# Kernel tuning notes

Measured on AMD Instinct MI355X. Metric: run time of the kernel, lower is better.

Reference implementation:

```python
import jax, jax.numpy as jnp
import numpy as np
import math

B, S, D, H = 4, 2048, 1024, 16
HD = D // H  # head_size = 64


def setup_inputs() -> dict:
    key = jax.random.key(0)
    ks = jax.random.split(key, 12)
    s = 1.0 / math.sqrt(D)
    inp = {
        "query_in": jax.random.normal(ks[0], (B, S, D), jnp.float32),
        "key_in": jax.random.normal(ks[1], (B, S, D), jnp.float32),
        "values_in": jax.random.normal(ks[2], (B, S, D), jnp.float32),
        # causal mask, broadcast over batch and heads
        "mask": jnp.tril(jnp.ones((S, S), jnp.int32))[None, None],
        "Wq": jax.random.normal(ks[3], (D, D), jnp.float32) * s,
        "bq": jnp.zeros((D,), jnp.float32),
        "Wk": jax.random.normal(ks[4], (D, D), jnp.float32) * s,
        "bk": jnp.zeros((D,), jnp.float32),
        "Wv": jax.random.normal(ks[5], (D, D), jnp.float32) * s,
        "bv": jnp.zeros((D,), jnp.float32),
        "Wo": jax.random.normal(ks[6], (D, D), jnp.float32) * s,
        "bo": jnp.zeros((D,), jnp.float32),
    }
    return inp


def _heads(x):
    # [B,S,D] -> [B,H,S,HD]
    return x.reshape(B, S, H, HD).transpose(0, 2, 1, 3)


def reference(query_in, key_in, values_in, mask, Wq, bq, Wk, bk, Wv, bv, Wo, bo):
    q = _heads(query_in @ Wq.T + bq)
    k = _heads(key_in @ Wk.T + bk)
    v = _heads(values_in @ Wv.T + bv)
    # scaled dot-product scores [B,H,Sq,Sk]
    att = jnp.einsum("bhqd,bhkd->bhqk", q, k) / math.sqrt(HD)
    att = jnp.where(mask == 0, jnp.float32(-1e9), att)
    # NOTE: original module applies dropout (identity at eval / p=0) directly
    # to scores with NO softmax -- faithfully reproduced here.
    out = jnp.einsum("bhqk,bhkd->bhqd", att, v)
    out = out.transpose(0, 2, 1, 3).reshape(B, S, D)
    return out @ Wo.T + bo
```

## Files before the change

### kernel.cpp

```cpp
#include <hip/hip_runtime.h>
#include <stdint.h>

typedef unsigned short ushort_t;
typedef __bf16 bf16x8 __attribute__((ext_vector_type(8)));
typedef float f32x4 __attribute__((ext_vector_type(4)));
typedef ushort_t us4 __attribute__((ext_vector_type(4)));

#define MFMA16(a, b, c) __builtin_amdgcn_mfma_f32_16x16x32_bf16((a), (b), (c), 0, 0, 0)

constexpr int Bn = 4, Sn = 2048, Dn = 1024, Hn = 16, HDn = 64;
constexpr float SCALE = 0.125f;
constexpr float NEG = -1e9f;

__device__ __forceinline__ float bf2f(ushort_t u) {
  unsigned x = ((unsigned)u) << 16;
  return __builtin_bit_cast(float, x);
}
__device__ __forceinline__ ushort_t f2bf(float f) {
  unsigned x = __builtin_bit_cast(unsigned, f);
  x = x + 0x7FFFu + ((x >> 16) & 1u);
  return (ushort_t)(x >> 16);
}
__device__ __forceinline__ uint4 ld8_f32_bf16(const float* __restrict__ p) {
  float4 a = *(const float4*)p;
  float4 b = *(const float4*)(p + 4);
  union { ushort_t u[8]; uint4 v; } r;
  r.u[0] = f2bf(a.x); r.u[1] = f2bf(a.y); r.u[2] = f2bf(a.z); r.u[3] = f2bf(a.w);
  r.u[4] = f2bf(b.x); r.u[5] = f2bf(b.y); r.u[6] = f2bf(b.z); r.u[7] = f2bf(b.w);
  return r.v;
}
__device__ __forceinline__ void gl2lds16(const void* g, void* l) {
  __builtin_amdgcn_global_load_lds(
      (__attribute__((address_space(1))) void*)g,
      (__attribute__((address_space(3))) void*)l, 16, 0, 0);
}

__global__ __launch_bounds__(256)
void cvt_all(const float* __restrict__ xq, const float* __restrict__ xk,
             const float* __restrict__ xv, const float* __restrict__ wq,
             const float* __restrict__ wk, const float* __restrict__ wv,
             const float* __restrict__ wo, ushort_t* __restrict__ Xd,
             ushort_t* __restrict__ Wd) {
  const int bid = blockIdx.x;
  if (bid < 12288) {
    const int which = bid >> 12;
    const float* s = which == 0 ? xq : which == 1 ? xk : xv;
    size_t i = ((size_t)(bid & 4095) * 256 + threadIdx.x) * 8;
    *(uint4*)(Xd + (size_t)which * 8388608 + i) = ld8_f32_bf16(s + i);
  } else {
    const int wb = bid - 12288, which = wb >> 9;
    const float* s = which == 0 ? wq : which == 1 ? wk : which == 2 ? wv : wo;
    size_t i = ((size_t)(wb & 511) * 256 + threadIdx.x) * 8;
    *(uint4*)(Wd + (size_t)which * 1048576 + i) = ld8_f32_bf16(s + i);
  }
}

__global__ __launch_bounds__(256, 4)
void gemm_qkv(const ushort_t* __restrict__ Xb, const ushort_t* __restrict__ Wb,
              const float* __restrict__ bq, const float* __restrict__ bk,
              const float* __restrict__ bv, ushort_t* __restrict__ Qd,
              ushort_t* __restrict__ Ktd, ushort_t* __restrict__ Vtd) {
  constexpr int K = 1024;
  __shared__ __align__(16) ushort_t As[128 * 64];
  __shared__ __align__(16) ushort_t Bs[128 * 64];

  const int z = blockIdx.z;
  const ushort_t* A  = Xb + (size_t)z * 8388608;
  const ushort_t* Wt = Wb + (size_t)z * 1048576;
  const float* bias = z == 0 ? bq : z == 1 ? bk : bv;
  ushort_t* Cp = z == 0 ? Qd : z == 1 ? Ktd : Vtd;

  const int tid = threadIdx.x;
  const int lane = tid & 63, w = tid >> 6;
  const int quad = lane >> 4, l16 = lane & 15;
  const int wm = w >> 1, wn = w & 1;
  const int row0 = blockIdx.x * 128;
  const int col0 = blockIdx.y * 128;

  const int sr = lane >> 3;
  const int sg = ((lane & 7) ^ (sr & 7)) * 8;
  const ushort_t* Ab = A  + (size_t)(row0 + w * 32 + sr) * K + sg;
  const ushort_t* Bb = Wt + (size_t)(col0 + w * 32 + sr) * K + sg;

  f32x4 acc[4][4] = {};

  for (int k0 = 0; k0 < K; k0 += 64) {
    __syncthreads();
#pragma unroll
    for (int i = 0; i < 4; ++i) {
      gl2lds16(Ab + (size_t)(i * 8) * K + k0, &As[(w * 32 + i * 8) * 64]);
      gl2lds16(Bb + (size_t)(i * 8) * K + k0, &Bs[(w * 32 + i * 8) * 64]);
    }
    __syncthreads();
#pragma unroll
    for (int ks = 0; ks < 2; ++ks) {
      const int kg = ((ks * 4 + quad) ^ (l16 & 7)) * 8;
      bf16x8 af[4], bfr[4];
#pragma unroll
      for (int mt = 0; mt < 4; ++mt)
        af[mt] = *(const bf16x8*)(&As[(wm * 64 + mt * 16 + l16) * 64 + kg]);
#pragma unroll
      for (int nt = 0; nt < 4; ++nt)
        bfr[nt] = *(const bf16x8*)(&Bs[(wn * 64 + nt * 16 + l16) * 64 + kg]);
#pragma unroll
      for (int mt = 0; mt < 4; ++mt)
#pragma unroll
        for (int nt = 0; nt < 4; ++nt)
          acc[mt][nt] = MFMA16(af[mt], bfr[nt], acc[mt][nt]);
    }
  }

#pragma unroll
  for (int mt = 0; mt < 4; ++mt) {
#pragma unroll
    for (int nt = 0; nt < 4; ++nt) {
      const int col = col0 + wn * 64 + nt * 16 + l16;
      const float bv4 = bias[col];
      const int rowb = row0 + wm * 64 + mt * 16 + quad * 4;
      if (z != 0) {
        const int b = rowb >> 11, s = rowb & (Sn - 1);
        const int h = col >> 6, hd = col & 63;
        us4 pk;
#pragma unroll
        for (int r = 0; r < 4; ++r) pk[r] = f2bf(acc[mt][nt][r] + bv4);
        *(us4*)(Cp + ((size_t)((b * Hn + h) * HDn + hd)) * Sn + s) = pk;
      } else {
#pragma unroll
        for (int r = 0; r < 4; ++r) {
          const int row = rowb + r;
          const int b = row >> 11, s = row & (Sn - 1);
          const int h = col >> 6, hd = col & 63;
          Cp[(((size_t)(b * Hn + h) * Sn + s) << 6) + hd] = f2bf(acc[mt][nt][r] + bv4);
        }
      }
    }
  }
}

__global__ __launch_bounds__(256, 4)
void gemm_out(const ushort_t* __restrict__ A, const ushort_t* __restrict__ Wt,
              const float* __restrict__ bias, float* __restrict__ Cp) {
  constexpr int K = 1024;
  __shared__ __align__(16) ushort_t As[128 * 64];
  __shared__ __align__(16) ushort_t Bs[128 * 64];

  const int tid = threadIdx.x;
  const int lane = tid & 63, w = tid >> 6;
  const int quad = lane >> 4, l16 = lane & 15;
  const int wm = w >> 1, wn = w & 1;
  const int row0 = blockIdx.x * 128;
  const int col0 = blockIdx.y * 128;

  const int sr = lane >> 3;
  const int sg = ((lane & 7) ^ (sr & 7)) * 8;
  const ushort_t* Ab = A  + (size_t)(row0 + w * 32 + sr) * K + sg;
  const ushort_t* Bb = Wt + (size_t)(col0 + w * 32 + sr) * K + sg;

  f32x4 acc[4][4] = {};

  for (int k0 = 0; k0 < K; k0 += 64) {
    __syncthreads();
#pragma unroll
    for (int i = 0; i < 4; ++i) {
      gl2lds16(Ab + (size_t)(i * 8) * K + k0, &As[(w * 32 + i * 8) * 64]);
      gl2lds16(Bb + (size_t)(i * 8) * K + k0, &Bs[(w * 32 + i * 8) * 64]);
    }
    __syncthreads();
#pragma unroll
    for (int ks = 0; ks < 2; ++ks) {
      const int kg = ((ks * 4 + quad) ^ (l16 & 7)) * 8;
      bf16x8 af[4], bfr[4];
#pragma unroll
      for (int mt = 0; mt < 4; ++mt)
        af[mt] = *(const bf16x8*)(&As[(wm * 64 + mt * 16 + l16) * 64 + kg]);
#pragma unroll
      for (int nt = 0; nt < 4; ++nt)
        bfr[nt] = *(const bf16x8*)(&Bs[(wn * 64 + nt * 16 + l16) * 64 + kg]);
#pragma unroll
      for (int mt = 0; mt < 4; ++mt)
#pragma unroll
        for (int nt = 0; nt < 4; ++nt)
          acc[mt][nt] = MFMA16(af[mt], bfr[nt], acc[mt][nt]);
    }
  }

#pragma unroll
  for (int mt = 0; mt < 4; ++mt)
#pragma unroll
    for (int nt = 0; nt < 4; ++nt) {
      const int col = col0 + wn * 64 + nt * 16 + l16;
      const float bv = bias[col];
      const int rowb = row0 + wm * 64 + mt * 16 + quad * 4;
#pragma unroll
      for (int r = 0; r < 4; ++r)
        Cp[(size_t)(rowb + r) * 1024 + col] = acc[mt][nt][r] + bv;
    }
}

__global__ __launch_bounds__(256)
void gtile(const ushort_t* __restrict__ Kt, const ushort_t* __restrict__ Vt,
           float* __restrict__ Gd, float* __restrict__ Rs) {
  __shared__ __align__(16) ushort_t Kts[4096];
  __shared__ __align__(16) ushort_t Vts[4096];
  __shared__ float tsum[64];
  const int tid = threadIdx.x, lane = tid & 63, w = tid >> 6;
  const int quad = lane >> 4, l16 = lane & 15;
  const int t = blockIdx.x, bh = blockIdx.y;
  const ushort_t* Ktb = Kt + (size_t)bh * HDn * Sn;
  const ushort_t* Vtb = Vt + (size_t)bh * HDn * Sn;

  const int sr = lane >> 3;
  const int sg = ((lane & 7) ^ (sr & 7)) * 8;

  if (tid < 64) tsum[tid] = 0.f;
#pragma unroll
  for (int c = 0; c < 2; ++c) {
    const int row = w * 16 + c * 8;
    gl2lds16(Ktb + (size_t)(row + sr) * Sn + t * 64 + sg, &Kts[row * 64]);
    gl2lds16(Vtb + (size_t)(row + sr) * Sn + t * 64 + sg, &Vts[row * 64]);
  }
  __syncthreads();

  f32x4 zacc[4] = {};
#pragma unroll
  for (int ks = 0; ks < 2; ++ks) {
    const int kg = ((ks * 4 + quad) ^ (l16 & 7)) * 8;
    bf16x8 ak = *(const bf16x8*)(&Kts[(w * 16 + l16) * 64 + kg]);
#pragma unroll
    for (int nt = 0; nt < 4; ++nt) {
      bf16x8 bv8 = *(const bf16x8*)(&Vts[(nt * 16 + l16) * 64 + kg]);
      zacc[nt] = MFMA16(ak, bv8, zacc[nt]);
    }
  }
  float* gd = Gd + (size_t)(bh * 32 + t) * 4096;
#pragma unroll
  for (int nt = 0; nt < 4; ++nt)
    *(f32x4*)(gd + (nt * 16 + l16) * 64 + w * 16 + quad * 4) = zacc[nt];

  {
    const int n = tid & 63, j = tid >> 6;
    float p = 0.f;
#pragma unroll
    for (int gg2 = 0; gg2 < 2; ++gg2) {
      const int g = 2 * j + gg2;
      union { uint4 v; ushort_t u[8]; } c;
      c.v = *(const uint4*)(&Vts[n * 64 + ((g ^ (n & 7)) << 3)]);
#pragma unroll
      for (int e = 0; e < 8; ++e) p += bf2f(c.u[e]);
    }
    atomicAdd(&tsum[n], p);
  }
  __syncthreads();
  if (tid < 64) Rs[(size_t)(bh * 32 + t) * 64 + tid] = tsum[tid];
}

__global__ __launch_bounds__(256)
void scan_attn(const ushort_t* __restrict__ Q, const ushort_t* __restrict__ Kt,
               const ushort_t* __restrict__ Vt, const float* __restrict__ Gd,
               const float* __restrict__ Rs, ushort_t* __restrict__ O) {
  __shared__ __align__(16) ushort_t Vts[2][4096];
  __shared__ __align__(16) ushort_t Zs[4096];
  __shared__ __align__(16) ushort_t Ks[4096];
  __shared__ __align__(16) ushort_t Ss[64][72];
  __shared__ __align__(16) float sfx[4][64];

  const int tid = threadIdx.x, lane = tid & 63, w = tid >> 6;
  const int quad = lane >> 4, l16 = lane & 15;
  const int bh = blockIdx.x;
  const int g = blockIdx.y;
  const int qt0 = g * 4;
  const int b = bh >> 4, h = bh & 15;
  const ushort_t* Qb  = Q  + (size_t)bh * Sn * HDn;
  const ushort_t* Ktb = Kt + (size_t)bh * HDn * Sn;
  const ushort_t* Vtb = Vt + (size_t)bh * HDn * Sn;
  const float* Gb = Gd + (size_t)bh * 32 * 4096;
  const float* Rb = Rs + (size_t)bh * 32 * 64;

  const int sr = lane >> 3;
  const int sg = ((lane & 7) ^ (sr & 7)) * 8;
  const int q8 = lane & 7, h8 = lane >> 3;

  const int zn = tid >> 2, zd0 = (tid & 3) * 16;
  const float* gthr = Gb + zn * 64 + zd0;

  uint4  kvr[2][2];
  bf16x8 bqr[2][2];
  f32x4  gq[2][4];

  {
    const int q0 = qt0 * 64;
#pragma unroll
    for (int c = 0; c < 2; ++c) {
      const int row = w * 16 + c * 8;
      gl2lds16(Vtb + (size_t)(row + sr) * Sn + q0 + sg, &Vts[0][row * 64]);
      kvr[0][c] = *(const uint4*)(Ktb + (size_t)(w * 16 + c * 8 + h8) * Sn + q0 + q8 * 8);
    }
#pragma unroll
    for (int ks = 0; ks < 2; ++ks)
      bqr[0][ks] = *(const bf16x8*)(Qb + (size_t)(q0 + w * 16 + l16) * HDn + (ks * 4 + quad) * 8);
#pragma unroll
    for (int j = 0; j < 4; ++j)
      gq[0][j] = *(const f32x4*)(gthr + (size_t)qt0 * 4096 + 4 * j);
  }

  if (tid < 64) {
    float acc = 0.f;
    for (int tau = 31; tau >= qt0; --tau) {
      if (tau < qt0 + 4) sfx[tau - qt0][tid] = acc;
      acc += Rb[(size_t)tau * 64 + tid];
    }
  }

  f32x4 Zacc[4] = {};
#pragma unroll 4
  for (int tau = 0; tau < qt0; ++tau) {
#pragma unroll
    for (int j = 0; j < 4; ++j)
      Zacc[j] += *(const f32x4*)(gthr + (size_t)tau * 4096 + 4 * j);
  }

#pragma unroll 4
  for (int i = 0; i < 4; ++i) {
    const int cur = i & 1;
    const int qt = qt0 + i, q0 = qt * 64;

    __syncthreads();

#pragma unroll
    for (int j = 0; j < 4; ++j) {
      const int d = zd0 + 4 * j;
      us4 pk;
#pragma unroll
      for (int r = 0; r < 4; ++r) pk[r] = f2bf(SCALE * Zacc[j][r]);
      *(us4*)(&Zs[zn * 64 + (((d >> 3) ^ (zn & 7)) << 3) + (d & 7)]) = pk;
    }
#pragma unroll
    for (int c = 0; c < 2; ++c) {
      const int hd = w * 16 + c * 8 + h8;
      const int G = hd >> 3;
      const ushort_t* ku = (const ushort_t*)&kvr[cur][c];
#pragma unroll
      for (int j = 0; j < 8; ++j) {
        const int e = (j + q8) & 7;
        const int s = q8 * 8 + e;
        Ks[s * 64 + ((G ^ e) << 3) + (hd & 7)] = ku[e];
      }
    }

    __syncthreads();

    if (i < 3) {
      const int q1 = (qt + 1) * 64, nxt = 1 - cur;
#pragma unroll
      for (int c = 0; c < 2; ++c) {
        const int row = w * 16 + c * 8;
        gl2lds16(Vtb + (size_t)(row + sr) * Sn + q1 + sg, &Vts[nxt][row * 64]);
        kvr[nxt][c] = *(const uint4*)(Ktb + (size_t)(w * 16 + c * 8 + h8) * Sn + q1 + q8 * 8);
      }
#pragma unroll
      for (int ks = 0; ks < 2; ++ks)
        bqr[nxt][ks] = *(const bf16x8*)(Qb + (size_t)(q1 + w * 16 + l16) * HDn + (ks * 4 + quad) * 8);
#pragma unroll
      for (int j = 0; j < 4; ++j)
        gq[nxt][j] = *(const f32x4*)(gthr + (size_t)(qt + 1) * 4096 + 4 * j);
    }

    f32x4 oacc[4] = {};
#pragma unroll
    for (int ks = 0; ks < 2; ++ks) {
      const int kg = ((ks * 4 + quad) ^ (l16 & 7)) * 8;
#pragma unroll
      for (int nt = 0; nt < 4; ++nt) {
        bf16x8 az = *(const bf16x8*)(&Zs[(nt * 16 + l16) * 64 + kg]);
        oacc[nt] = MFMA16(az, bqr[cur][ks], oacc[nt]);
      }
    }
    f32x4 sacc[4] = {};
#pragma unroll
    for (int ks = 0; ks < 2; ++ks) {
      const int kg = ((ks * 4 + quad) ^ (l16 & 7)) * 8;
#pragma unroll
      for (int nt = 0; nt < 4; ++nt) {
        bf16x8 ak = *(const bf16x8*)(&Ks[(nt * 16 + l16) * 64 + kg]);
        sacc[nt] = MFMA16(ak, bqr[cur][ks], sacc[nt]);
      }
    }
    const int qrel = w * 16 + l16;
#pragma unroll
    for (int nt = 0; nt < 4; ++nt) {
      const int kb = nt * 16 + quad * 4;
      us4 pk;
#pragma unroll
      for (int r = 0; r < 4; ++r) {
        float val = (kb + r > qrel) ? NEG : sacc[nt][r] * SCALE;
        pk[r] = f2bf(val);
      }
      *(us4*)(&Ss[qrel][kb]) = pk;
    }
#pragma unroll
    for (int ks = 0; ks < 2; ++ks) {
      bf16x8 bs = *(const bf16x8*)(&Ss[qrel][ks * 32 + quad * 8]);
#pragma unroll
      for (int nt = 0; nt < 4; ++nt) {
        bf16x8 av = *(const bf16x8*)(&Vts[cur][(nt * 16 + l16) * 64 + (((ks * 4 + quad) ^ (l16 & 7)) << 3)]);
        oacc[nt] = MFMA16(av, bs, oacc[nt]);
      }
    }

    const int s = q0 + w * 16 + l16;
#pragma unroll
    for (int nt = 0; nt < 4; ++nt) {
      const int nb = nt * 16 + quad * 4;
      float4 s4 = *(const float4*)(&sfx[i][nb]);
      us4 pk;
      pk[0] = f2bf(oacc[nt][0] + NEG * s4.x);
      pk[1] = f2bf(oacc[nt][1] + NEG * s4.y);
      pk[2] = f2bf(oacc[nt][2] + NEG * s4.z);
      pk[3] = f2bf(oacc[nt][3] + NEG * s4.w);
      *(us4*)(&O[((size_t)(b * Sn + s)) * Dn + h * 64 + nb]) = pk;
    }

#pragma unroll
    for (int j = 0; j < 4; ++j) Zacc[j] += gq[cur][j];
  }
}

extern "C" void kernel_launch(void* const* d_in, const int* in_sizes, int n_in,
                              void* d_out, int out_size, void* d_ws, size_t ws_size,
                              hipStream_t stream) {
  const float* Xq = (const float*)d_in[0];
  const float* Xk = (const float*)d_in[1];
  const float* Xv = (const float*)d_in[2];
  const float* Wq = (const float*)d_in[4];
  const float* bq = (const float*)d_in[5];
  const float* Wk = (const float*)d_in[6];
  const float* bk = (const float*)d_in[7];
  const float* Wv = (const float*)d_in[8];
  const float* bv = (const float*)d_in[9];
  const float* Wo = (const float*)d_in[10];
  const float* bo = (const float*)d_in[11];

  constexpr size_t MiB = 1024 * 1024;
  char* ws = (char*)d_ws;
  ushort_t* Xb  = (ushort_t*)(ws);
  ushort_t* Wb  = (ushort_t*)(ws + 48 * MiB);
  ushort_t* Qb  = (ushort_t*)(ws + 56 * MiB);
  ushort_t* Ktb = (ushort_t*)(ws + 72 * MiB);
  ushort_t* Vtb = (ushort_t*)(ws + 88 * MiB);
  ushort_t* Ob  = (ushort_t*)(ws + 120 * MiB);
  float*    Gd  = (float*)   (ws + 144 * MiB);
  float*    Rsum= (float*)   (ws + 176 * MiB);

  cvt_all<<<14336, 256, 0, stream>>>(Xq, Xk, Xv, Wq, Wk, Wv, Wo, Xb, Wb);
  gemm_qkv<<<dim3(64, 8, 3), 256, 0, stream>>>(Xb, Wb, bq, bk, bv, Qb, Ktb, Vtb);
  gtile<<<dim3(32, 64), 256, 0, stream>>>(Ktb, Vtb, Gd, Rsum);
  scan_attn<<<dim3(64, 8), 256, 0, stream>>>(Qb, Ktb, Vtb, Gd, Rsum, Ob);
  gemm_out<<<dim3(64, 8), 256, 0, stream>>>(Ob, Wb + (size_t)3 * 1048576, bo,
                                            (float*)d_out);
}
```

Before: 303.5 us.

## Fuse fp32-to-bf16 activation conversion into QKV GEMM tile loads

Removes the separate conversion pass over the three fp32 activation tensors. The QKV GEMM now loads fp32 tiles straight into LDS with an XOR swizzle and converts them to bf16 when it reads the MFMA operands. A weights-only conversion kernel remains. This avoids writing and re-reading a 48 MiB bf16 intermediate. In exchange the GEMM doubles LDS use for A and global traffic per tile (fp32, re-read by each of the 8 column blocks), which may reduce occupancy.

```diff
diff --git a/kernel.cpp b/kernel.cpp
--- a/kernel.cpp
+++ b/kernel.cpp
@@ -20,6 +20,12 @@
   unsigned x = __builtin_bit_cast(unsigned, f);
   x = x + 0x7FFFu + ((x >> 16) & 1u);
   return (ushort_t)(x >> 16);
+}
+__device__ __forceinline__ bf16x8 cvt8(f32x4 a, f32x4 b) {
+  bf16x8 r;
+  r[0] = (__bf16)a[0]; r[1] = (__bf16)a[1]; r[2] = (__bf16)a[2]; r[3] = (__bf16)a[3];
+  r[4] = (__bf16)b[0]; r[5] = (__bf16)b[1]; r[6] = (__bf16)b[2]; r[7] = (__bf16)b[3];
+  return r;
 }
 __device__ __forceinline__ uint4 ld8_f32_bf16(const float* __restrict__ p) {
   float4 a = *(const float4*)p;
@@ -36,36 +42,27 @@
 }
 
 __global__ __launch_bounds__(256)
-void cvt_all(const float* __restrict__ xq, const float* __restrict__ xk,
-             const float* __restrict__ xv, const float* __restrict__ wq,
-             const float* __restrict__ wk, const float* __restrict__ wv,
-             const float* __restrict__ wo, ushort_t* __restrict__ Xd,
-             ushort_t* __restrict__ Wd) {
-  const int bid = blockIdx.x;
-  if (bid < 12288) {
-    const int which = bid >> 12;
-    const float* s = which == 0 ? xq : which == 1 ? xk : xv;
-    size_t i = ((size_t)(bid & 4095) * 256 + threadIdx.x) * 8;
-    *(uint4*)(Xd + (size_t)which * 8388608 + i) = ld8_f32_bf16(s + i);
-  } else {
-    const int wb = bid - 12288, which = wb >> 9;
-    const float* s = which == 0 ? wq : which == 1 ? wk : which == 2 ? wv : wo;
-    size_t i = ((size_t)(wb & 511) * 256 + threadIdx.x) * 8;
-    *(uint4*)(Wd + (size_t)which * 1048576 + i) = ld8_f32_bf16(s + i);
-  }
+void cvt_w(const float* __restrict__ wq, const float* __restrict__ wk,
+           const float* __restrict__ wv, const float* __restrict__ wo,
+           ushort_t* __restrict__ Wd) {
+  const int wb = blockIdx.x, which = wb >> 9;
+  const float* s = which == 0 ? wq : which == 1 ? wk : which == 2 ? wv : wo;
+  size_t i = ((size_t)(wb & 511) * 256 + threadIdx.x) * 8;
+  *(uint4*)(Wd + (size_t)which * 1048576 + i) = ld8_f32_bf16(s + i);
 }
 
 __global__ __launch_bounds__(256, 4)
-void gemm_qkv(const ushort_t* __restrict__ Xb, const ushort_t* __restrict__ Wb,
+void gemm_qkv(const float* __restrict__ xq, const float* __restrict__ xk,
+              const float* __restrict__ xv, const ushort_t* __restrict__ Wb,
               const float* __restrict__ bq, const float* __restrict__ bk,
               const float* __restrict__ bv, ushort_t* __restrict__ Qd,
               ushort_t* __restrict__ Ktd, ushort_t* __restrict__ Vtd) {
   constexpr int K = 1024;
-  __shared__ __align__(16) ushort_t As[128 * 64];
+  __shared__ __align__(16) float    Asf[128 * 64];
   __shared__ __align__(16) ushort_t Bs[128 * 64];
 
   const int z = blockIdx.z;
-  const ushort_t* A  = Xb + (size_t)z * 8388608;
+  const float* A = z == 0 ? xq : z == 1 ? xk : xv;
   const ushort_t* Wt = Wb + (size_t)z * 1048576;
   const float* bias = z == 0 ? bq : z == 1 ? bk : bv;
   ushort_t* Cp = z == 0 ? Qd : z == 1 ? Ktd : Vtd;
@@ -79,26 +76,38 @@
 
   const int sr = lane >> 3;
   const int sg = ((lane & 7) ^ (sr & 7)) * 8;
-  const ushort_t* Ab = A  + (size_t)(row0 + w * 32 + sr) * K + sg;
   const ushort_t* Bb = Wt + (size_t)(col0 + w * 32 + sr) * K + sg;
 
+  const int rq4 = lane >> 4;
+  const int gsl = lane & 15;
+
   f32x4 acc[4][4] = {};
 
   for (int k0 = 0; k0 < K; k0 += 64) {
     __syncthreads();
 #pragma unroll
-    for (int i = 0; i < 4; ++i) {
-      gl2lds16(Ab + (size_t)(i * 8) * K + k0, &As[(w * 32 + i * 8) * 64]);
+    for (int i = 0; i < 4; ++i)
       gl2lds16(Bb + (size_t)(i * 8) * K + k0, &Bs[(w * 32 + i * 8) * 64]);
+#pragma unroll
+    for (int i = 0; i < 8; ++i) {
+      const int lr4 = w * 32 + i * 4;
+      const int lr = lr4 + rq4;
+      const int psrc = gsl ^ (lr & 15);
+      gl2lds16(A + (size_t)(row0 + lr) * K + k0 + (psrc << 2), &Asf[lr4 * 64]);
     }
     __syncthreads();
 #pragma unroll
     for (int ks = 0; ks < 2; ++ks) {
       const int kg = ((ks * 4 + quad) ^ (l16 & 7)) * 8;
+      const int p0 = (ks * 4 + quad) * 2;
+      const int s0 = ((p0 ^ l16) << 2), s1 = (((p0 ^ l16) ^ 1) << 2);
       bf16x8 af[4], bfr[4];
 #pragma unroll
-      for (int mt = 0; mt < 4; ++mt)
-        af[mt] = *(const bf16x8*)(&As[(wm * 64 + mt * 16 + l16) * 64 + kg]);
+      for (int mt = 0; mt < 4; ++mt) {
+        const int rb = (wm * 64 + mt * 16 + l16) * 64;
+        af[mt] = cvt8(*(const f32x4*)(&Asf[rb + s0]),
+                      *(const f32x4*)(&Asf[rb + s1]));
+      }
 #pragma unroll
       for (int nt = 0; nt < 4; ++nt)
         bfr[nt] = *(const bf16x8*)(&Bs[(wn * 64 + nt * 16 + l16) * 64 + kg]);
@@ -442,7 +451,6 @@
 
   constexpr size_t MiB = 1024 * 1024;
   char* ws = (char*)d_ws;
-  ushort_t* Xb  = (ushort_t*)(ws);
   ushort_t* Wb  = (ushort_t*)(ws + 48 * MiB);
   ushort_t* Qb  = (ushort_t*)(ws + 56 * MiB);
   ushort_t* Ktb = (ushort_t*)(ws + 72 * MiB);
@@ -451,8 +459,9 @@
   float*    Gd  = (float*)   (ws + 144 * MiB);
   float*    Rsum= (float*)   (ws + 176 * MiB);
 
-  cvt_all<<<14336, 256, 0, stream>>>(Xq, Xk, Xv, Wq, Wk, Wv, Wo, Xb, Wb);
-  gemm_qkv<<<dim3(64, 8, 3), 256, 0, stream>>>(Xb, Wb, bq, bk, bv, Qb, Ktb, Vtb);
+  cvt_w<<<2048, 256, 0, stream>>>(Wq, Wk, Wv, Wo, Wb);
+  gemm_qkv<<<dim3(64, 8, 3), 256, 0, stream>>>(Xq, Xk, Xv, Wb, bq, bk, bv,
+                                               Qb, Ktb, Vtb);
   gtile<<<dim3(32, 64), 256, 0, stream>>>(Ktb, Vtb, Gd, Rsum);
   scan_attn<<<dim3(64, 8), 256, 0, stream>>>(Qb, Ktb, Vtb, Gd, Rsum, Ob);
   gemm_out<<<dim3(64, 8), 256, 0, stream>>>(Ob, Wb + (size_t)3 * 1048576, bo,
```

Measured after the change: 307.0 us. Within noise of the previous version (+1.1%).

## Fuse gtile, scan_attn and output GEMM into one persistent kernel with grid barriers

Applied to the files above, without the earlier changes.

Merges the three tail kernels into a single 512-block persistent kernel that runs the per-tile K^T V products, the prefix-scan attention, and the output projection in sequence, separated by software grid barriers built on atomics. A shared LDS buffer is reused across the three phases. The aim is to remove two kernel launch gaps and the tail/drain effects between dependent launches. In exchange it adds global-atomic barrier cost, forces a launch bound of 2 blocks per CU, and depends on all 512 blocks being resident at once, otherwise the barrier deadlocks.

```diff
diff --git a/kernel.cpp b/kernel.cpp
--- a/kernel.cpp
+++ b/kernel.cpp
@@ -11,6 +11,7 @@
 constexpr int Bn = 4, Sn = 2048, Dn = 1024, Hn = 16, HDn = 64;
 constexpr float SCALE = 0.125f;
 constexpr float NEG = -1e9f;
+constexpr unsigned NBLK = 512;
 
 __device__ __forceinline__ float bf2f(ushort_t u) {
   unsigned x = ((unsigned)u) << 16;
@@ -33,6 +34,23 @@
   __builtin_amdgcn_global_load_lds(
       (__attribute__((address_space(1))) void*)g,
       (__attribute__((address_space(3))) void*)l, 16, 0, 0);
+}
+
+__device__ __forceinline__ void gridbar(unsigned* cnt, unsigned* gen) {
+  __threadfence();
+  __syncthreads();
+  if (threadIdx.x == 0) {
+    unsigned g = atomicAdd(gen, 0u);
+    if (atomicAdd(cnt, 1u) == NBLK - 1) {
+      atomicExch(cnt, 0u);
+      __threadfence();
+      atomicAdd(gen, 1u);
+    } else {
+      while (atomicAdd(gen, 0u) == g) __builtin_amdgcn_s_sleep(8);
+    }
+  }
+  __syncthreads();
+  __threadfence();
 }
 
 __global__ __launch_bounds__(256)
@@ -137,291 +155,286 @@
   }
 }
 
-__global__ __launch_bounds__(256, 4)
-void gemm_out(const ushort_t* __restrict__ A, const ushort_t* __restrict__ Wt,
-              const float* __restrict__ bias, float* __restrict__ Cp) {
-  constexpr int K = 1024;
-  __shared__ __align__(16) ushort_t As[128 * 64];
-  __shared__ __align__(16) ushort_t Bs[128 * 64];
-
-  const int tid = threadIdx.x;
-  const int lane = tid & 63, w = tid >> 6;
-  const int quad = lane >> 4, l16 = lane & 15;
-  const int wm = w >> 1, wn = w & 1;
-  const int row0 = blockIdx.x * 128;
-  const int col0 = blockIdx.y * 128;
-
-  const int sr = lane >> 3;
-  const int sg = ((lane & 7) ^ (sr & 7)) * 8;
-  const ushort_t* Ab = A  + (size_t)(row0 + w * 32 + sr) * K + sg;
-  const ushort_t* Bb = Wt + (size_t)(col0 + w * 32 + sr) * K + sg;
-
-  f32x4 acc[4][4] = {};
-
-  for (int k0 = 0; k0 < K; k0 += 64) {
-    __syncthreads();
-#pragma unroll
-    for (int i = 0; i < 4; ++i) {
-      gl2lds16(Ab + (size_t)(i * 8) * K + k0, &As[(w * 32 + i * 8) * 64]);
-      gl2lds16(Bb + (size_t)(i * 8) * K + k0, &Bs[(w * 32 + i * 8) * 64]);
-    }
-    __syncthreads();
-#pragma unroll
-    for (int ks = 0; ks < 2; ++ks) {
-      const int kg = ((ks * 4 + quad) ^ (l16 & 7)) * 8;
-      bf16x8 af[4], bfr[4];
-#pragma unroll
-      for (int mt = 0; mt < 4; ++mt)
-        af[mt] = *(const bf16x8*)(&As[(wm * 64 + mt * 16 + l16) * 64 + kg]);
-#pragma unroll
-      for (int nt = 0; nt < 4; ++nt)
-        bfr[nt] = *(const bf16x8*)(&Bs[(wn * 64 + nt * 16 + l16) * 64 + kg]);
-#pragma unroll
-      for (int mt = 0; mt < 4; ++mt)
-#pragma unroll
-        for (int nt = 0; nt < 4; ++nt)
-          acc[mt][nt] = MFMA16(af[mt], bfr[nt], acc[mt][nt]);
-    }
-  }
-
-#pragma unroll
-  for (int mt = 0; mt < 4; ++mt)
-#pragma unroll
-    for (int nt = 0; nt < 4; ++nt) {
-      const int col = col0 + wn * 64 + nt * 16 + l16;
-      const float bv = bias[col];
-      const int rowb = row0 + wm * 64 + mt * 16 + quad * 4;
-#pragma unroll
-      for (int r = 0; r < 4; ++r)
-        Cp[(size_t)(rowb + r) * 1024 + col] = acc[mt][nt][r] + bv;
-    }
-}
-
-__global__ __launch_bounds__(256)
-void gtile(const ushort_t* __restrict__ Kt, const ushort_t* __restrict__ Vt,
-           float* __restrict__ Gd, float* __restrict__ Rs) {
-  __shared__ __align__(16) ushort_t Kts[4096];
-  __shared__ __align__(16) ushort_t Vts[4096];
-  __shared__ float tsum[64];
+__global__ __launch_bounds__(256, 2)
+void tail_fused(const ushort_t* __restrict__ Q, const ushort_t* __restrict__ Kt,
+                const ushort_t* __restrict__ Vt, float* __restrict__ Gd,
+                float* __restrict__ Rs, ushort_t* __restrict__ O,
+                const ushort_t* __restrict__ Wo, const float* __restrict__ bo,
+                float* __restrict__ Cout, unsigned* __restrict__ bar) {
+  __shared__ __align__(16) char smem[43008];
+
   const int tid = threadIdx.x, lane = tid & 63, w = tid >> 6;
   const int quad = lane >> 4, l16 = lane & 15;
-  const int t = blockIdx.x, bh = blockIdx.y;
-  const ushort_t* Ktb = Kt + (size_t)bh * HDn * Sn;
-  const ushort_t* Vtb = Vt + (size_t)bh * HDn * Sn;
-
-  const int sr = lane >> 3;
-  const int sg = ((lane & 7) ^ (sr & 7)) * 8;
-
-  if (tid < 64) tsum[tid] = 0.f;
-#pragma unroll
-  for (int c = 0; c < 2; ++c) {
-    const int row = w * 16 + c * 8;
-    gl2lds16(Ktb + (size_t)(row + sr) * Sn + t * 64 + sg, &Kts[row * 64]);
-    gl2lds16(Vtb + (size_t)(row + sr) * Sn + t * 64 + sg, &Vts[row * 64]);
-  }
-  __syncthreads();
-
-  f32x4 zacc[4] = {};
-#pragma unroll
-  for (int ks = 0; ks < 2; ++ks) {
-    const int kg = ((ks * 4 + quad) ^ (l16 & 7)) * 8;
-    bf16x8 ak = *(const bf16x8*)(&Kts[(w * 16 + l16) * 64 + kg]);
-#pragma unroll
-    for (int nt = 0; nt < 4; ++nt) {
-      bf16x8 bv8 = *(const bf16x8*)(&Vts[(nt * 16 + l16) * 64 + kg]);
-      zacc[nt] = MFMA16(ak, bv8, zacc[nt]);
-    }
-  }
-  float* gd = Gd + (size_t)(bh * 32 + t) * 4096;
-#pragma unroll
-  for (int nt = 0; nt < 4; ++nt)
-    *(f32x4*)(gd + (nt * 16 + l16) * 64 + w * 16 + quad * 4) = zacc[nt];
-
-  {
-    const int n = tid & 63, j = tid >> 6;
-    float p = 0.f;
-#pragma unroll
-    for (int gg2 = 0; gg2 < 2; ++gg2) {
-      const int g = 2 * j + gg2;
-      union { uint4 v; ushort_t u[8]; } c;
-      c.v = *(const uint4*)(&Vts[n * 64 + ((g ^ (n & 7)) << 3)]);
-#pragma unroll
-      for (int e = 0; e < 8; ++e) p += bf2f(c.u[e]);
-    }
-    atomicAdd(&tsum[n], p);
-  }
-  __syncthreads();
-  if (tid < 64) Rs[(size_t)(bh * 32 + t) * 64 + tid] = tsum[tid];
-}
-
-__global__ __launch_bounds__(256)
-void scan_attn(const ushort_t* __restrict__ Q, const ushort_t* __restrict__ Kt,
-               const ushort_t* __restrict__ Vt, const float* __restrict__ Gd,
-               const float* __restrict__ Rs, ushort_t* __restrict__ O) {
-  __shared__ __align__(16) ushort_t Vts[2][4096];
-  __shared__ __align__(16) ushort_t Zs[4096];
-  __shared__ __align__(16) ushort_t Ks[4096];
-  __shared__ __align__(16) ushort_t Ss[64][72];
-  __shared__ __align__(16) float sfx[4][64];
-
-  const int tid = threadIdx.x, lane = tid & 63, w = tid >> 6;
-  const int quad = lane >> 4, l16 = lane & 15;
-  const int bh = blockIdx.x;
-  const int g = blockIdx.y;
-  const int qt0 = g * 4;
+  const int beta = blockIdx.x;
+  const int bh = beta & 63, tq = beta >> 6;
   const int b = bh >> 4, h = bh & 15;
-  const ushort_t* Qb  = Q  + (size_t)bh * Sn * HDn;
-  const ushort_t* Ktb = Kt + (size_t)bh * HDn * Sn;
-  const ushort_t* Vtb = Vt + (size_t)bh * HDn * Sn;
-  const float* Gb = Gd + (size_t)bh * 32 * 4096;
-  const float* Rb = Rs + (size_t)bh * 32 * 64;
-
   const int sr = lane >> 3;
   const int sg = ((lane & 7) ^ (sr & 7)) * 8;
   const int q8 = lane & 7, h8 = lane >> 3;
 
-  const int zn = tid >> 2, zd0 = (tid & 3) * 16;
-  const float* gthr = Gb + zn * 64 + zd0;
-
-  uint4  kvr[2][2];
-  bf16x8 bqr[2][2];
-  f32x4  gq[2][4];
+  const ushort_t* Ktb = Kt + (size_t)bh * HDn * Sn;
+  const ushort_t* Vtb = Vt + (size_t)bh * HDn * Sn;
 
   {
-    const int q0 = qt0 * 64;
-#pragma unroll
-    for (int c = 0; c < 2; ++c) {
-      const int row = w * 16 + c * 8;
-      gl2lds16(Vtb + (size_t)(row + sr) * Sn + q0 + sg, &Vts[0][row * 64]);
-      kvr[0][c] = *(const uint4*)(Ktb + (size_t)(w * 16 + c * 8 + h8) * Sn + q0 + q8 * 8);
-    }
-#pragma unroll
-    for (int ks = 0; ks < 2; ++ks)
-      bqr[0][ks] = *(const bf16x8*)(Qb + (size_t)(q0 + w * 16 + l16) * HDn + (ks * 4 + quad) * 8);
-#pragma unroll
-    for (int j = 0; j < 4; ++j)
-      gq[0][j] = *(const f32x4*)(gthr + (size_t)qt0 * 4096 + 4 * j);
-  }
-
-  if (tid < 64) {
-    float acc = 0.f;
-    for (int tau = 31; tau >= qt0; --tau) {
-      if (tau < qt0 + 4) sfx[tau - qt0][tid] = acc;
-      acc += Rb[(size_t)tau * 64 + tid];
-    }
-  }
-
-  f32x4 Zacc[4] = {};
-#pragma unroll 4
-  for (int tau = 0; tau < qt0; ++tau) {
-#pragma unroll
-    for (int j = 0; j < 4; ++j)
-      Zacc[j] += *(const f32x4*)(gthr + (size_t)tau * 4096 + 4 * j);
-  }
-
-#pragma unroll 4
-  for (int i = 0; i < 4; ++i) {
-    const int cur = i & 1;
-    const int qt = qt0 + i, q0 = qt * 64;
-
-    __syncthreads();
-
-#pragma unroll
+    ushort_t* Kts = (ushort_t*)smem;
+    ushort_t* VtsS = (ushort_t*)(smem + 8192);
+    float* tsum = (float*)(smem + 16384);
+#pragma unroll 1
     for (int j = 0; j < 4; ++j) {
-      const int d = zd0 + 4 * j;
-      us4 pk;
-#pragma unroll
-      for (int r = 0; r < 4; ++r) pk[r] = f2bf(SCALE * Zacc[j][r]);
-      *(us4*)(&Zs[zn * 64 + (((d >> 3) ^ (zn & 7)) << 3) + (d & 7)]) = pk;
-    }
-#pragma unroll
-    for (int c = 0; c < 2; ++c) {
-      const int hd = w * 16 + c * 8 + h8;
-      const int G = hd >> 3;
-      const ushort_t* ku = (const ushort_t*)&kvr[cur][c];
-#pragma unroll
-      for (int j = 0; j < 8; ++j) {
-        const int e = (j + q8) & 7;
-        const int s = q8 * 8 + e;
-        Ks[s * 64 + ((G ^ e) << 3) + (hd & 7)] = ku[e];
-      }
-    }
-
-    __syncthreads();
-
-    if (i < 3) {
-      const int q1 = (qt + 1) * 64, nxt = 1 - cur;
+      const int t = tq * 4 + j;
+      __syncthreads();
+      if (tid < 64) tsum[tid] = 0.f;
 #pragma unroll
       for (int c = 0; c < 2; ++c) {
         const int row = w * 16 + c * 8;
-        gl2lds16(Vtb + (size_t)(row + sr) * Sn + q1 + sg, &Vts[nxt][row * 64]);
-        kvr[nxt][c] = *(const uint4*)(Ktb + (size_t)(w * 16 + c * 8 + h8) * Sn + q1 + q8 * 8);
+        gl2lds16(Ktb + (size_t)(row + sr) * Sn + t * 64 + sg, &Kts[row * 64]);
+        gl2lds16(Vtb + (size_t)(row + sr) * Sn + t * 64 + sg, &VtsS[row * 64]);
+      }
+      __syncthreads();
+      f32x4 zacc[4] = {};
+#pragma unroll
+      for (int ks = 0; ks < 2; ++ks) {
+        const int kg = ((ks * 4 + quad) ^ (l16 & 7)) * 8;
+        bf16x8 ak = *(const bf16x8*)(&Kts[(w * 16 + l16) * 64 + kg]);
+#pragma unroll
+        for (int nt = 0; nt < 4; ++nt) {
+          bf16x8 bv8 = *(const bf16x8*)(&VtsS[(nt * 16 + l16) * 64 + kg]);
+          zacc[nt] = MFMA16(ak, bv8, zacc[nt]);
+        }
+      }
+      float* gd = Gd + (size_t)(bh * 32 + t) * 4096;
+#pragma unroll
+      for (int nt = 0; nt < 4; ++nt)
+        *(f32x4*)(gd + (nt * 16 + l16) * 64 + w * 16 + quad * 4) = zacc[nt];
+      {
+        const int n = tid & 63, jj = tid >> 6;
+        float p = 0.f;
+#pragma unroll
+        for (int gg2 = 0; gg2 < 2; ++gg2) {
+          const int g2 = 2 * jj + gg2;
+          union { uint4 v; ushort_t u[8]; } cc;
+          cc.v = *(const uint4*)(&VtsS[n * 64 + ((g2 ^ (n & 7)) << 3)]);
+#pragma unroll
+          for (int e = 0; e < 8; ++e) p += bf2f(cc.u[e]);
+        }
+        atomicAdd(&tsum[n], p);
+      }
+      __syncthreads();
+      if (tid < 64) Rs[(size_t)(bh * 32 + t) * 64 + tid] = tsum[tid];
+    }
+  }
+
+  gridbar(bar, bar + 1);
+
+  {
+    ushort_t* Vts = (ushort_t*)smem;
+    ushort_t* Zs = (ushort_t*)(smem + 16384);
+    ushort_t* Ks = (ushort_t*)(smem + 24576);
+    ushort_t (*Ss)[72] = (ushort_t(*)[72])(smem + 32768);
+    float (*sfx)[64] = (float(*)[64])(smem + 41984);
+
+    const int g = tq;
+    const int qt0 = g * 4;
+    const ushort_t* Qb = Q + (size_t)bh * Sn * HDn;
+    const float* Gb = Gd + (size_t)bh * 32 * 4096;
+    const float* Rb = Rs + (size_t)bh * 32 * 64;
+
+    const int zn = tid >> 2, zd0 = (tid & 3) * 16;
+    const float* gthr = Gb + zn * 64 + zd0;
+
+    uint4  kvr[2][2];
+    bf16x8 bqr[2][2];
+    f32x4  gq[2][4];
+
+    {
+      const int q0 = qt0 * 64;
+#pragma unroll
+      for (int c = 0; c < 2; ++c) {
+        const int row = w * 16 + c * 8;
+        gl2lds16(Vtb + (size_t)(row + sr) * Sn + q0 + sg, &Vts[row * 64]);
+        kvr[0][c] = *(const uint4*)(Ktb + (size_t)(w * 16 + c * 8 + h8) * Sn + q0 + q8 * 8);
       }
 #pragma unroll
       for (int ks = 0; ks < 2; ++ks)
-        bqr[nxt][ks] = *(const bf16x8*)(Qb + (size_t)(q1 + w * 16 + l16) * HDn + (ks * 4 + quad) * 8);
+        bqr[0][ks] = *(const bf16x8*)(Qb + (size_t)(q0 + w * 16 + l16) * HDn + (ks * 4 + quad) * 8);
 #pragma unroll
       for (int j = 0; j < 4; ++j)
-        gq[nxt][j] = *(const f32x4*)(gthr + (size_t)(qt + 1) * 4096 + 4 * j);
-    }
-
-    f32x4 oacc[4] = {};
-#pragma unroll
-    for (int ks = 0; ks < 2; ++ks) {
-      const int kg = ((ks * 4 + quad) ^ (l16 & 7)) * 8;
+        gq[0][j] = *(const f32x4*)(gthr + (size_t)qt0 * 4096 + 4 * j);
+    }
+
+    if (tid < 64) {
+      float acc = 0.f;
+      for (int tau = 31; tau >= qt0; --tau) {
+        if (tau < qt0 + 4) sfx[tau - qt0][tid] = acc;
+        acc += Rb[(size_t)tau * 64 + tid];
+      }
+    }
+
+    f32x4 Zacc[4] = {};
+#pragma unroll 4
+    for (int tau = 0; tau < qt0; ++tau) {
+#pragma unroll
+      for (int j = 0; j < 4; ++j)
+        Zacc[j] += *(const f32x4*)(gthr + (size_t)tau * 4096 + 4 * j);
+    }
+
+#pragma unroll 4
+    for (int i = 0; i < 4; ++i) {
+      const int cur = i & 1;
+      const int qt = qt0 + i, q0 = qt * 64;
+
+      __syncthreads();
+
+#pragma unroll
+      for (int j = 0; j < 4; ++j) {
+        const int d = zd0 + 4 * j;
+        us4 pk;
+#pragma unroll
+        for (int r = 0; r < 4; ++r) pk[r] = f2bf(SCALE * Zacc[j][r]);
+        *(us4*)(&Zs[zn * 64 + (((d >> 3) ^ (zn & 7)) << 3) + (d & 7)]) = pk;
+      }
+#pragma unroll
+      for (int c = 0; c < 2; ++c) {
+        const int hd = w * 16 + c * 8 + h8;
+        const int G = hd >> 3;
+        const ushort_t* ku = (const ushort_t*)&kvr[cur][c];
+#pragma unroll
+        for (int j = 0; j < 8; ++j) {
+          const int e = (j + q8) & 7;
+          const int s = q8 * 8 + e;
+          Ks[s * 64 + ((G ^ e) << 3) + (hd & 7)] = ku[e];
+        }
+      }
+
+      __syncthreads();
+
+      if (i < 3) {
+        const int q1 = (qt + 1) * 64, nxt = 1 - cur;
+#pragma unroll
+        for (int c = 0; c < 2; ++c) {
+          const int row = w * 16 + c * 8;
+          gl2lds16(Vtb + (size_t)(row + sr) * Sn + q1 + sg, &Vts[nxt * 4096 + row * 64]);
+          kvr[nxt][c] = *(const uint4*)(Ktb + (size_t)(w * 16 + c * 8 + h8) * Sn + q1 + q8 * 8);
+        }
+#pragma unroll
+        for (int ks = 0; ks < 2; ++ks)
+          bqr[nxt][ks] = *(const bf16x8*)(Qb + (size_t)(q1 + w * 16 + l16) * HDn + (ks * 4 + quad) * 8);
+#pragma unroll
+        for (int j = 0; j < 4; ++j)
+          gq[nxt][j] = *(const f32x4*)(gthr + (size_t)(qt + 1) * 4096 + 4 * j);
+      }
+
+      f32x4 oacc[4] = {};
+#pragma unroll
+      for (int ks = 0; ks < 2; ++ks) {
+        const int kg = ((ks * 4 + quad) ^ (l16 & 7)) * 8;
+#pragma unroll
+        for (int nt = 0; nt < 4; ++nt) {
+          bf16x8 az = *(const bf16x8*)(&Zs[(nt * 16 + l16) * 64 + kg]);
+          oacc[nt] = MFMA16(az, bqr[cur][ks], oacc[nt]);
+        }
+      }
+      f32x4 sacc[4] = {};
+#pragma unroll
+      for (int ks = 0; ks < 2; ++ks) {
+        const int kg = ((ks * 4 + quad) ^ (l16 & 7)) * 8;
+#pragma unroll
+        for (int nt = 0; nt < 4; ++nt) {
+          bf16x8 ak = *(const bf16x8*)(&Ks[(nt * 16 + l16) * 64 + kg]);
+          sacc[nt] = MFMA16(ak, bqr[cur][ks], sacc[nt]);
+        }
+      }
+      const int qrel = w * 16 + l16;
 #pragma unroll
       for (int nt = 0; nt < 4; ++nt) {
-        bf16x8 az = *(const bf16x8*)(&Zs[(nt * 16 + l16) * 64 + kg]);
-        oacc[nt] = MFMA16(az, bqr[cur][ks], oacc[nt]);
-      }
-    }
-    f32x4 sacc[4] = {};
-#pragma unroll
-    for (int ks = 0; ks < 2; ++ks) {
-      const int kg = ((ks * 4 + quad) ^ (l16 & 7)) * 8;
+        const int kb = nt * 16 + quad * 4;
+        us4 pk;
+#pragma unroll
+        for (int r = 0; r < 4; ++r) {
+          float val = (kb + r > qrel) ? NEG : sacc[nt][r] * SCALE;
+          pk[r] = f2bf(val);
+        }
+        *(us4*)(&Ss[qrel][kb]) = pk;
+      }
+#pragma unroll
+      for (int ks = 0; ks < 2; ++ks) {
+        bf16x8 bs = *(const bf16x8*)(&Ss[qrel][ks * 32 + quad * 8]);
+#pragma unroll
+        for (int nt = 0; nt < 4; ++nt) {
+          bf16x8 av = *(const bf16x8*)(&Vts[cur * 4096 + (nt * 16 + l16) * 64 + (((ks * 4 + quad) ^ (l16 & 7)) << 3)]);
+          oacc[nt] = MFMA16(av, bs, oacc[nt]);
+        }
+      }
+
+      const int s = q0 + w * 16 + l16;
 #pragma unroll
       for (int nt = 0; nt < 4; ++nt) {
-        bf16x8 ak = *(const bf16x8*)(&Ks[(nt * 16 + l16) * 64 + kg]);
-        sacc[nt] = MFMA16(ak, bqr[cur][ks], sacc[nt]);
-      }
-    }
-    const int qrel = w * 16 + l16;
-#pragma unroll
-    for (int nt = 0; nt < 4; ++nt) {
-      const int kb = nt * 16 + quad * 4;
-      us4 pk;
-#pragma unroll
-      for (int r = 0; r < 4; ++r) {
-        float val = (kb + r > qrel) ? NEG : sacc[nt][r] * SCALE;
-        pk[r] = f2bf(val);
-      }
-      *(us4*)(&Ss[qrel][kb]) = pk;
-    }
-#pragma unroll
-    for (int ks = 0; ks < 2; ++ks) {
-      bf16x8 bs = *(const bf16x8*)(&Ss[qrel][ks * 32 + quad * 8]);
+        const int nb = nt * 16 + quad * 4;
+        float4 s4 = *(const float4*)(&sfx[i][nb]);
+        us4 pk;
+        pk[0] = f2bf(oacc[nt][0] + NEG * s4.x);
+        pk[1] = f2bf(oacc[nt][1] + NEG * s4.y);
+        pk[2] = f2bf(oacc[nt][2] + NEG * s4.z);
+        pk[3] = f2bf(oacc[nt][3] + NEG * s4.w);
+        *(us4*)(&O[((size_t)(b * Sn + s)) * Dn + h * 64 + nb]) = pk;
+      }
+
+#pragma unroll
+      for (int j = 0; j < 4; ++j) Zacc[j] += gq[cur][j];
+    }
+  }
+
+  gridbar(bar, bar + 1);
+
+  {
+    constexpr int K = 1024;
+    ushort_t* As = (ushort_t*)smem;
+    ushort_t* Bs = (ushort_t*)(smem + 16384);
+    const int wm = w >> 1, wn = w & 1;
+    const int row0 = bh * 128;
+    const int col0 = tq * 128;
+    const ushort_t* Ab = O  + (size_t)(row0 + w * 32 + sr) * K + sg;
+    const ushort_t* Bb = Wo + (size_t)(col0 + w * 32 + sr) * K + sg;
+
+    f32x4 acc[4][4] = {};
+
+    for (int k0 = 0; k0 < K; k0 += 64) {
+      __syncthreads();
+#pragma unroll
+      for (int i = 0; i < 4; ++i) {
+        gl2lds16(Ab + (size_t)(i * 8) * K + k0, &As[(w * 32 + i * 8) * 64]);
+        gl2lds16(Bb + (size_t)(i * 8) * K + k0, &Bs[(w * 32 + i * 8) * 64]);
+      }
+      __syncthreads();
+#pragma unroll
+      for (int ks = 0; ks < 2; ++ks) {
+        const int kg = ((ks * 4 + quad) ^ (l16 & 7)) * 8;
+        bf16x8 af[4], bfr[4];
+#pragma unroll
+        for (int mt = 0; mt < 4; ++mt)
+          af[mt] = *(const bf16x8*)(&As[(wm * 64 + mt * 16 + l16) * 64 + kg]);
+#pragma unroll
+        for (int nt = 0; nt < 4; ++nt)
+          bfr[nt] = *(const bf16x8*)(&Bs[(wn * 64 + nt * 16 + l16) * 64 + kg]);
+#pragma unroll
+        for (int mt = 0; mt < 4; ++mt)
+#pragma unroll
+          for (int nt = 0; nt < 4; ++nt)
+            acc[mt][nt] = MFMA16(af[mt], bfr[nt], acc[mt][nt]);
+      }
+    }
+
+#pragma unroll
+    for (int mt = 0; mt < 4; ++mt)
 #pragma unroll
       for (int nt = 0; nt < 4; ++nt) {
-        bf16x8 av = *(const bf16x8*)(&Vts[cur][(nt * 16 + l16) * 64 + (((ks * 4 + quad) ^ (l16 & 7)) << 3)]);
-        oacc[nt] = MFMA16(av, bs, oacc[nt]);
-      }
-    }
-
-    const int s = q0 + w * 16 + l16;
-#pragma unroll
-    for (int nt = 0; nt < 4; ++nt) {
-      const int nb = nt * 16 + quad * 4;
-      float4 s4 = *(const float4*)(&sfx[i][nb]);
-      us4 pk;
-      pk[0] = f2bf(oacc[nt][0] + NEG * s4.x);
-      pk[1] = f2bf(oacc[nt][1] + NEG * s4.y);
-      pk[2] = f2bf(oacc[nt][2] + NEG * s4.z);
-      pk[3] = f2bf(oacc[nt][3] + NEG * s4.w);
-      *(us4*)(&O[((size_t)(b * Sn + s)) * Dn + h * 64 + nb]) = pk;
-    }
-
-#pragma unroll
-    for (int j = 0; j < 4; ++j) Zacc[j] += gq[cur][j];
+        const int col = col0 + wn * 64 + nt * 16 + l16;
+        const float bv = bo[col];
+        const int rowb = row0 + wm * 64 + mt * 16 + quad * 4;
+#pragma unroll
+        for (int r = 0; r < 4; ++r)
+          Cout[(size_t)(rowb + r) * 1024 + col] = acc[mt][nt][r] + bv;
+      }
   }
 }
 
@@ -450,11 +463,13 @@
   ushort_t* Ob  = (ushort_t*)(ws + 120 * MiB);
   float*    Gd  = (float*)   (ws + 144 * MiB);
   float*    Rsum= (float*)   (ws + 176 * MiB);
+  unsigned* bar = (unsigned*)(ws + 200 * MiB);
+
+  hipMemsetAsync(bar, 0, 64, stream);
 
   cvt_all<<<14336, 256, 0, stream>>>(Xq, Xk, Xv, Wq, Wk, Wv, Wo, Xb, Wb);
   gemm_qkv<<<dim3(64, 8, 3), 256, 0, stream>>>(Xb, Wb, bq, bk, bv, Qb, Ktb, Vtb);
-  gtile<<<dim3(32, 64), 256, 0, stream>>>(Ktb, Vtb, Gd, Rsum);
-  scan_attn<<<dim3(64, 8), 256, 0, stream>>>(Qb, Ktb, Vtb, Gd, Rsum, Ob);
-  gemm_out<<<dim3(64, 8), 256, 0, stream>>>(Ob, Wb + (size_t)3 * 1048576, bo,
-                                            (float*)d_out);
-}
+  tail_fused<<<512, 256, 0, stream>>>(Qb, Ktb, Vtb, Gd, Rsum, Ob,
+                                      Wb + (size_t)3 * 1048576, bo,
+                                      (float*)d_out, bar);
+}
```

New measurement: 533.7 us. +75.8%, slower.
